# Kernel optimization log

Measured on AMD Instinct MI355X. Metric: run time of the kernel, lower is better.

## Reference

```python
import jax, jax.numpy as jnp
import numpy as np

B, S, D, H, WS = 2, 4096, 768, 12, 256
HD = D // H
NW = S // WS
EPS = 1e-5


def layernorm(x, g, b):
    mu = jnp.mean(x, axis=-1, keepdims=True)
    var = jnp.mean(jnp.square(x - mu), axis=-1, keepdims=True)
    return (x - mu) * jax.lax.rsqrt(var + EPS) * g + b


def setup_inputs() -> dict:
    key = jax.random.key(0)
    ks = jax.random.split(key, 8)
    s = 0.02
    return {
        "x": jax.random.normal(ks[0], (B, S, D), dtype=jnp.float32),
        "Wq": jax.random.normal(ks[1], (D, D), dtype=jnp.float32) * s,
        "bq": jnp.zeros((D,), jnp.float32),
        "Wk": jax.random.normal(ks[2], (D, D), dtype=jnp.float32) * s,
        "bk": jnp.zeros((D,), jnp.float32),
        "Wv": jax.random.normal(ks[3], (D, D), dtype=jnp.float32) * s,
        "bv": jnp.zeros((D,), jnp.float32),
        "Wo": jax.random.normal(ks[4], (D, D), dtype=jnp.float32) * s,
        "bo": jnp.zeros((D,), jnp.float32),
        "ln1_g": jnp.ones((D,), jnp.float32),
        "ln1_b": jnp.zeros((D,), jnp.float32),
        "W1": jax.random.normal(ks[5], (D, 4 * D), dtype=jnp.float32) * s,
        "b1": jnp.zeros((4 * D,), jnp.float32),
        "W2": jax.random.normal(ks[6], (4 * D, D), dtype=jnp.float32) * s,
        "b2": jnp.zeros((D,), jnp.float32),
        "ln2_g": jnp.ones((D,), jnp.float32),
        "ln2_b": jnp.zeros((D,), jnp.float32),
    }


def _attn(h, Wq, bq, Wk, bk, Wv, bv, Wo, bo):
    q = (h @ Wq + bq).reshape(B, S, H, HD)
    k = (h @ Wk + bk).reshape(B, S, H, HD)
    v = (h @ Wv + bv).reshape(B, S, H, HD)
    # split into windows: [B, NW, WS, H, HD]
    kb = k.reshape(B, NW, WS, H, HD)
    vb = v.reshape(B, NW, WS, H, HD)
    qw = jnp.moveaxis(q.reshape(B, NW, WS, H, HD), 1, 0)  # [NW, B, WS, H, HD]
    inv = 1.0 / np.sqrt(HD).astype(np.float32)

    def step(carry, qi_i):
        qi, i = qi_i  # qi: [B, WS, H, HD]
        # per key-window scores: [B, H, NW, WSq, WSk]
        scores = jnp.einsum('bqhd,bjkhd->bhjqk', qi, kb) * inv
        attn = jax.nn.softmax(scores, axis=-1)  # per-block softmax (as in source)
        mask = (jnp.arange(NW) <= i).astype(attn.dtype)  # block-causal, include own window
        attn = attn * mask[None, None, :, None, None]
        ctx = jnp.einsum('bhjqk,bjkhd->bqhd', attn, vb)  # sum over key windows
        return carry, ctx

    _, ctxs = jax.lax.scan(step, None, (qw, jnp.arange(NW)))
    ctx = jnp.moveaxis(ctxs, 0, 1).reshape(B, S, D)
    return ctx @ Wo + bo


def reference(x, Wq, bq, Wk, bk, Wv, bv, Wo, bo, ln1_g, ln1_b, W1, b1, W2, b2, ln2_g, ln2_b):
    attn_out = _attn(layernorm(x, ln1_g, ln1_b), Wq, bq, Wk, bk, Wv, bv, Wo, bo)
    x = x + attn_out
    h2 = layernorm(x, ln2_g, ln2_b)
    ff = jax.nn.gelu(h2 @ W1 + b1, approximate=False) @ W2 + b2
    return x + ff
```

## Files before the change

kernel.cpp:

```cpp
#include <hip/hip_runtime.h>
#include <cstdint>
#include <cstddef>

#define DEV __device__ __forceinline__

typedef unsigned short u16;
typedef unsigned int u32;
typedef __attribute__((ext_vector_type(8))) short s16x8;
typedef __attribute__((ext_vector_type(4))) float f32x4;
typedef __attribute__((ext_vector_type(4))) unsigned int u32x4;

typedef unsigned int u32_as1 __attribute__((address_space(1)));
typedef unsigned int u32_as3 __attribute__((address_space(3)));

DEV u16 f2bf(float f){
  unsigned u = __float_as_uint(f);
  u += 0x7fffu + ((u >> 16) & 1u);
  return (u16)(u >> 16);
}

DEV u32 cvtpk_bf16(float lo, float hi){
  u32 r;
  asm("v_cvt_pk_bf16_f32 %0, %1, %2" : "=v"(r) : "v"(lo), "v"(hi));
  return r;
}

DEV float fexp2(float x){
  float r;
  asm("v_exp_f32 %0, %1" : "=v"(r) : "v"(x));
  return r;
}

DEV float frcp(float x){
  float r;
  asm("v_rcp_f32 %0, %1" : "=v"(r) : "v"(x));
  return r;
}

DEV void gload16(const void* g, void* l){
  __builtin_amdgcn_global_load_lds((const u32_as1*)g, (u32_as3*)l, 16, 0, 0);
}

DEV float gelu_tanh(float x){
  float x2 = x*x;
  float z = 2.3022083f * x * fmaf(x2, 0.044715f, 1.0f);
  z = fminf(z, 100.0f);
  float t = fexp2(z);
  return x * t * frcp(t + 1.0f);
}

template<int NZ>
__global__ __launch_bounds__(256) void wconv_kernel(
    const float* __restrict__ Wa, const float* __restrict__ Wb,
    const float* __restrict__ Wc, const float* __restrict__ Wd,
    u16* __restrict__ Da, u16* __restrict__ Db, u16* __restrict__ Dc, u16* __restrict__ Dd,
    int K, int N){
  __shared__ float tl[32][33];
  int z = (NZ>1) ? blockIdx.z : 0;
  const float* W = (z==0)?Wa:(z==1)?Wb:(z==2)?Wc:Wd;
  u16* Wt = (z==0)?Da:(z==1)?Db:(z==2)?Dc:Dd;
  int tx = threadIdx.x & 31, ty = threadIdx.x >> 5;
  int k0 = blockIdx.x * 32, n0 = blockIdx.y * 32;
  #pragma unroll
  for (int p=0;p<4;p++)
    tl[ty+8*p][tx] = W[(size_t)(k0+ty+8*p)*N + (n0+tx)];
  __syncthreads();
  #pragma unroll
  for (int p=0;p<4;p++){
    int n = ty+8*p;
    Wt[(size_t)(n0+n)*K + (k0+tx)] = f2bf(tl[tx][n]);
  }
}

__global__ __launch_bounds__(256) void ln_kernel(const float* __restrict__ x,
                                                 const float* __restrict__ g,
                                                 const float* __restrict__ bta,
                                                 u16* __restrict__ out){
  int row = blockIdx.x, t = threadIdx.x;
  const float* xr = x + (size_t)row*768;
  float v0 = xr[t], v1 = xr[t+256], v2 = xr[t+512];
  float s = v0+v1+v2, s2 = v0*v0+v1*v1+v2*v2;
  #pragma unroll
  for (int m=1;m<64;m<<=1){ s += __shfl_xor(s,m); s2 += __shfl_xor(s2,m); }
  __shared__ float ls[4], ls2[4];
  int w = t>>6;
  if ((t&63)==0){ ls[w]=s; ls2[w]=s2; }
  __syncthreads();
  s = ls[0]+ls[1]+ls[2]+ls[3]; s2 = ls2[0]+ls2[1]+ls2[2]+ls2[3];
  float mu = s*(1.0f/768.0f);
  float rstd = rsqrtf(s2*(1.0f/768.0f) - mu*mu + 1e-5f);
  u16* orow = out + (size_t)row*768;
  orow[t]     = f2bf((v0-mu)*rstd*g[t]     + bta[t]);
  orow[t+256] = f2bf((v1-mu)*rstd*g[t+256] + bta[t+256]);
  orow[t+512] = f2bf((v2-mu)*rstd*g[t+512] + bta[t+512]);
}

template<bool GELU, bool RES, bool OUTBF16, int BM, bool VPERM=false>
__global__ __launch_bounds__(256) void gemm_kernel(
    const u16* __restrict__ A, const u16* __restrict__ Bt0, size_t btStride,
    const float* __restrict__ bias0, const float* __restrict__ bias1, const float* __restrict__ bias2,
    const float* __restrict__ res, void* __restrict__ out0, size_t outStride,
    int M, int N, int K, float qscale, u32* __restrict__ vtb = nullptr)
{
  constexpr int AM = BM/32;
  __shared__ u16 As[BM*64];
  __shared__ u16 Bs[128*64];
  const int t = threadIdx.x, lane = t & 63, w = t >> 6;
  const int lj = lane & 15, g = lane >> 4;
  const int wm = w >> 1, wn = w & 1;
  const int z = blockIdx.z;
  const u16* Bt = Bt0 + (size_t)z * btStride;
  const float* bias = (z==0) ? bias0 : (z==1 ? bias1 : bias2);
  const u16* Arow = A  + (size_t)blockIdx.x * BM * K;
  const u16* Brow = Bt + (size_t)blockIdx.y * 128 * K;

  f32x4 acc[AM][4];
  #pragma unroll
  for (int a=0;a<AM;a++)
    #pragma unroll
    for (int b=0;b<4;b++){ f32x4 zz = {0.f,0.f,0.f,0.f}; acc[a][b] = zz; }

  for (int kk=0; kk<K; kk+=64){
    #pragma unroll
    for (int cc=0;cc<BM/32;cc++){
      int c = cc*256 + t;
      int row = c>>3, gp = c&7;
      gload16(Arow + (size_t)row*K + kk + ((gp ^ (row&7))<<3),
              (void*)(As + (size_t)(cc*256 + w*64)*8));
    }
    #pragma unroll
    for (int cc=0;cc<4;cc++){
      int c = cc*256 + t;
      int row = c>>3, gp = c&7;
      gload16(Brow + (size_t)row*K + kk + ((gp ^ (row&7))<<3),
              (void*)(Bs + (size_t)(cc*256 + w*64)*8));
    }
    __syncthreads();
    #pragma unroll
    for (int ks=0;ks<2;ks++){
      s16x8 af[AM], bfr[4];
      #pragma unroll
      for (int mt=0;mt<AM;mt++){
        int row = wm*(BM/2)+mt*16+lj;
        af[mt]  = *(const s16x8*)&As[(size_t)row*64 + (((ks*4+g) ^ (lj&7))<<3)];
      }
      #pragma unroll
      for (int nt=0;nt<4;nt++){
        int row = wn*64+nt*16+lj;
        bfr[nt] = *(const s16x8*)&Bs[(size_t)row*64 + (((ks*4+g) ^ (lj&7))<<3)];
      }
      #pragma unroll
      for (int mt=0;mt<AM;mt++)
        #pragma unroll
        for (int nt=0;nt<4;nt++)
          acc[mt][nt] = __builtin_amdgcn_mfma_f32_16x16x32_bf16(af[mt], bfr[nt], acc[mt][nt], 0,0,0);
    }
    __syncthreads();
  }

  const size_t gr0 = (size_t)blockIdx.x*BM + wm*(BM/2);
  const int gc0 = blockIdx.y*128 + wn*64;

  if (VPERM && z == 2){
    const int b_ = (int)(gr0 >> 12);
    const int kt = (int)((gr0 & 4095) >> 6);
    #pragma unroll
    for (int mt2=0; mt2<AM; mt2+=2){
      const u32 gnq = 4*(mt2>>1) + g;
      #pragma unroll
      for (int nt=0;nt<4;nt++){
        int gc = gc0 + nt*16 + lj;
        int hh = gc>>6, dd = gc&63;
        float bv = bias[gc];
        size_t base = ((size_t)(b_*12+hh)*64 + dd)*2048 + (size_t)kt*32 + gnq*4;
        #pragma unroll
        for (int r=0;r<4;r++){
          float ve = acc[mt2][nt][r]   + bv;
          float vo = acc[mt2+1][nt][r] + bv;
          vtb[base + r] = cvtpk_bf16(ve, vo);
        }
      }
    }
    return;
  }

  float* outF = (float*)out0; u16* outB = (u16*)out0;
  if (OUTBF16) outB += (size_t)z*outStride; else outF += (size_t)z*outStride;
  #pragma unroll
  for (int mt=0;mt<AM;mt++)
    #pragma unroll
    for (int nt=0;nt<4;nt++){
      int gc = gc0 + nt*16 + lj;
      float bv = bias[gc];
      #pragma unroll
      for (int r=0;r<4;r++){
        size_t gr = gr0 + mt*16 + g*4 + r;
        float val = acc[mt][nt][r] + bv;
        if (z==0) val *= qscale;
        if (RES)  val += res[gr*(size_t)N + gc];
        if (GELU) val = gelu_tanh(val);
        if (OUTBF16) outB[gr*(size_t)N + gc] = f2bf(val);
        else         outF[gr*(size_t)N + gc] = val;
      }
    }
}

__global__ __launch_bounds__(256,2) void attn_kernel(
    const u16* __restrict__ qb, const u16* __restrict__ kb,
    const u16* __restrict__ vtb, u16* __restrict__ ctx)
{
  __shared__ u16 Ks[256*64];
  __shared__ u16 Vs[64*256];
  const int t = threadIdx.x, lane = t & 63, w = t >> 6;
  const int lj = lane & 15, g = lane >> 4;
  const int bx = blockIdx.x;
  const int pp = bx & 7, qq = (bx >> 3) & 3, bh = bx >> 5;
  const int h = bh % 12, b = bh / 12;
  const size_t seqbase = (size_t)b * 4096;
  const int hoff = h * 64;

  #pragma unroll
  for (int f=0; f<2; f++){
    const int iw = f ? (15 - pp) : pp;
    const int qrow0 = iw*256 + qq*64 + w*16;

    s16x8 qa[2];
    #pragma unroll
    for (int ks=0;ks<2;ks++)
      qa[ks] = *(const s16x8*)(qb + (seqbase + qrow0 + lj)*768 + hoff + ks*32 + g*8);

    f32x4 cacc[4];
    #pragma unroll
    for (int dt=0;dt<4;dt++){ f32x4 zz = {0.f,0.f,0.f,0.f}; cacc[dt] = zz; }

    for (int jw=0; jw<=iw; jw++){
      const u16* kwin = kb + (seqbase + jw*256)*768 + hoff;
      const u16* vtwin = vtb + (size_t)bh*64*4096 + jw*256;

      __syncthreads();
      #pragma unroll
      for (int cc=0;cc<8;cc++){
        int c = cc*256 + t;
        int krow = c>>3, vp = c&7;
        gload16(kwin + (size_t)krow*768 + ((vp ^ (krow&7))<<3),
                (void*)(Ks + (size_t)(cc*256 + w*64)*8));
      }
      #pragma unroll
      for (int cc=0;cc<8;cc++){
        int c = cc*256 + t;
        int d = c>>5, cp = c&31;
        gload16(vtwin + (size_t)d*4096 + ((cp ^ (d&15))<<3),
                (void*)(Vs + (size_t)(cc*256 + w*64)*8));
      }
      __syncthreads();

      f32x4 sacc[16];
      #pragma unroll
      for (int kt=0;kt<16;kt++){ f32x4 zz = {0.f,0.f,0.f,0.f}; sacc[kt] = zz; }
      __builtin_amdgcn_s_setprio(1);
      #pragma unroll
      for (int kt=0;kt<16;kt++){
        int kl = kt*16 + lj;
        #pragma unroll
        for (int ks=0;ks<2;ks++){
          s16x8 kf = *(const s16x8*)&Ks[ (size_t)kl*64 + (((4*ks+g) ^ (kl&7))<<3) ];
          sacc[kt] = __builtin_amdgcn_mfma_f32_16x16x32_bf16(kf, qa[ks], sacc[kt], 0,0,0);
        }
      }
      __builtin_amdgcn_s_setprio(0);

      float sm = 0.f;
      #pragma unroll
      for (int kt=0;kt<16;kt++)
        #pragma unroll
        for (int r=0;r<4;r++){
          float pv = fexp2(sacc[kt][r]);
          sacc[kt][r] = pv; sm += pv;
        }
      sm += __shfl_xor(sm, 16);
      sm += __shfl_xor(sm, 32);
      float rs = frcp(sm);

      f32x4 pacc[4];
      #pragma unroll
      for (int dt=0;dt<4;dt++){ f32x4 zz = {0.f,0.f,0.f,0.f}; pacc[dt] = zz; }
      #pragma unroll
      for (int ks=0;ks<8;ks++){
        u32x4 pw;
        #pragma unroll
        for (int r=0;r<4;r++)
          pw[r] = cvtpk_bf16(sacc[2*ks][r], sacc[2*ks+1][r]);
        s16x8 pa = __builtin_bit_cast(s16x8, pw);
        __builtin_amdgcn_s_setprio(1);
        #pragma unroll
        for (int dt=0;dt<4;dt++){
          int d = dt*16 + lj;
          s16x8 vf = *(const s16x8*)&Vs[ (size_t)d*256 + (((4*ks+g) ^ (d&15))<<3) ];
          pacc[dt] = __builtin_amdgcn_mfma_f32_16x16x32_bf16(pa, vf, pacc[dt], 0,0,0);
        }
        __builtin_amdgcn_s_setprio(0);
      }
      #pragma unroll
      for (int dt=0;dt<4;dt++)
        #pragma unroll
        for (int r=0;r<4;r++)
          cacc[dt][r] += rs * pacc[dt][r];
    }

    #pragma unroll
    for (int dt=0;dt<4;dt++)
      #pragma unroll
      for (int r=0;r<4;r++){
        int qrow = qrow0 + g*4 + r;
        ctx[ (seqbase + qrow)*768 + hoff + dt*16 + lj ] = f2bf(cacc[dt][r]);
      }
  }
}

extern "C" void kernel_launch(void* const* d_in, const int* in_sizes, int n_in,
                              void* d_out, int out_size, void* d_ws, size_t ws_size,
                              hipStream_t stream)
{
  const float* x    = (const float*)d_in[0];
  const float* Wq   = (const float*)d_in[1];
  const float* bq   = (const float*)d_in[2];
  const float* Wk   = (const float*)d_in[3];
  const float* bk   = (const float*)d_in[4];
  const float* Wv   = (const float*)d_in[5];
  const float* bv   = (const float*)d_in[6];
  const float* Wo   = (const float*)d_in[7];
  const float* bo   = (const float*)d_in[8];
  const float* ln1g = (const float*)d_in[9];
  const float* ln1b = (const float*)d_in[10];
  const float* W1   = (const float*)d_in[11];
  const float* b1   = (const float*)d_in[12];
  const float* W2   = (const float*)d_in[13];
  const float* b2   = (const float*)d_in[14];
  const float* ln2g = (const float*)d_in[15];
  const float* ln2b = (const float*)d_in[16];

  char* ws = (char*)d_ws;
  constexpr size_t SZ_W768  = (size_t)768*768*2;
  constexpr size_t SZ_W3072 = (size_t)768*3072*2;
  constexpr size_t SZ_HB    = (size_t)8192*768*2;
  u16* wtq = (u16*)(ws);
  u16* wtk = (u16*)(ws + SZ_W768);
  u16* wtv = (u16*)(ws + 2*SZ_W768);
  u16* wto = (u16*)(ws + 3*SZ_W768);
  u16* wt1 = (u16*)(ws + 4*SZ_W768);
  u16* wt2 = (u16*)(ws + 4*SZ_W768 + SZ_W3072);
  char* p0 = ws + 4*SZ_W768 + 2*SZ_W3072;
  u16*   hbuf  = (u16*)p0;
  u16*   qbuf  = (u16*)(p0 + SZ_HB);
  u16*   kbuf  = (u16*)(p0 + 2*SZ_HB);
  u16*   vtbuf = (u16*)(p0 + 3*SZ_HB);
  u16*   cbuf  = (u16*)(p0 + 4*SZ_HB);
  float* x1    = (float*)(p0 + 5*SZ_HB);
  u16*   ffa   = qbuf;
  float* outp  = (float*)d_out;

  wconv_kernel<4><<<dim3(24,24,4), 256, 0, stream>>>(
      Wq, Wk, Wv, Wo, wtq, wtk, wtv, wto, 768, 768);
  wconv_kernel<1><<<dim3(24,96), 256, 0, stream>>>(
      W1, W1, W1, W1, wt1, wt1, wt1, wt1, 768, 3072);
  wconv_kernel<1><<<dim3(96,24), 256, 0, stream>>>(
      W2, W2, W2, W2, wt2, wt2, wt2, wt2, 3072, 768);

  ln_kernel<<<8192, 256, 0, stream>>>(x, ln1g, ln1b, hbuf);
  gemm_kernel<false,false,true,128,true><<<dim3(64,6,3), 256, 0, stream>>>(
      hbuf, wtq, (size_t)768*768, bq, bk, bv, nullptr, qbuf, (size_t)8192*768,
      8192, 768, 768, 0.180336880111f, (u32*)vtbuf);
  attn_kernel<<<768, 256, 0, stream>>>(qbuf, kbuf, vtbuf, cbuf);
  gemm_kernel<false,true,false,64><<<dim3(128,6,1), 256, 0, stream>>>(
      cbuf, wto, 0, bo, bo, bo, x, x1, 0, 8192, 768, 768, 1.0f);
  ln_kernel<<<8192, 256, 0, stream>>>(x1, ln2g, ln2b, hbuf);
  gemm_kernel<true,false,true,128><<<dim3(64,24,1), 256, 0, stream>>>(
      hbuf, wt1, 0, b1, b1, b1, nullptr, ffa, 0, 8192, 3072, 768, 1.0f);
  gemm_kernel<false,true,false,64><<<dim3(128,6,1), 256, 0, stream>>>(
      ffa, wt2, 0, b2, b2, b2, x1, outp, 0, 8192, 768, 3072, 1.0f);
}
```

Before: 296.4 us.

## Share one LDS buffer for K and V in attention and store residual in bf16

The attention kernel now keeps K and V in a single 32 KB LDS buffer instead of two. V is loaded only after the QK^T MFMAs finish, with extra barriers between phases, and the launch bound is raised to 3 blocks per CU so occupancy can go up. Separately, the post-attention residual x1 is stored as bf16 instead of fp32, and the second layernorm and the final residual add read it as bf16, which halves that tensor's memory traffic. In exchange, the V load can no longer overlap the score computation, and the residual stream loses precision, which may increase numerical error.

```diff
diff --git a/kernel.cpp b/kernel.cpp
--- a/kernel.cpp
+++ b/kernel.cpp
@@ -18,6 +18,8 @@
   u += 0x7fffu + ((u >> 16) & 1u);
   return (u16)(u >> 16);
 }
+
+DEV float bf2f(u16 v){ return __uint_as_float(((u32)v) << 16); }
 
 DEV u32 cvtpk_bf16(float lo, float hi){
   u32 r;
@@ -72,13 +74,20 @@
   }
 }
 
-__global__ __launch_bounds__(256) void ln_kernel(const float* __restrict__ x,
+template<bool INBF16>
+__global__ __launch_bounds__(256) void ln_kernel(const void* __restrict__ xin,
                                                  const float* __restrict__ g,
                                                  const float* __restrict__ bta,
                                                  u16* __restrict__ out){
   int row = blockIdx.x, t = threadIdx.x;
-  const float* xr = x + (size_t)row*768;
-  float v0 = xr[t], v1 = xr[t+256], v2 = xr[t+512];
+  float v0, v1, v2;
+  if (INBF16){
+    const u16* xr = (const u16*)xin + (size_t)row*768;
+    v0 = bf2f(xr[t]); v1 = bf2f(xr[t+256]); v2 = bf2f(xr[t+512]);
+  } else {
+    const float* xr = (const float*)xin + (size_t)row*768;
+    v0 = xr[t]; v1 = xr[t+256]; v2 = xr[t+512];
+  }
   float s = v0+v1+v2, s2 = v0*v0+v1*v1+v2*v2;
   #pragma unroll
   for (int m=1;m<64;m<<=1){ s += __shfl_xor(s,m); s2 += __shfl_xor(s2,m); }
@@ -95,11 +104,11 @@
   orow[t+512] = f2bf((v2-mu)*rstd*g[t+512] + bta[t+512]);
 }
 
-template<bool GELU, bool RES, bool OUTBF16, int BM, bool VPERM=false>
+template<bool GELU, bool RES, bool OUTBF16, int BM, bool VPERM=false, bool RESBF16=false>
 __global__ __launch_bounds__(256) void gemm_kernel(
     const u16* __restrict__ A, const u16* __restrict__ Bt0, size_t btStride,
     const float* __restrict__ bias0, const float* __restrict__ bias1, const float* __restrict__ bias2,
-    const float* __restrict__ res, void* __restrict__ out0, size_t outStride,
+    const void* __restrict__ res, void* __restrict__ out0, size_t outStride,
     int M, int N, int K, float qscale, u32* __restrict__ vtb = nullptr)
 {
   constexpr int AM = BM/32;
@@ -197,7 +206,10 @@
         size_t gr = gr0 + mt*16 + g*4 + r;
         float val = acc[mt][nt][r] + bv;
         if (z==0) val *= qscale;
-        if (RES)  val += res[gr*(size_t)N + gc];
+        if (RES){
+          if (RESBF16) val += bf2f(((const u16*)res)[gr*(size_t)N + gc]);
+          else         val += ((const float*)res)[gr*(size_t)N + gc];
+        }
         if (GELU) val = gelu_tanh(val);
         if (OUTBF16) outB[gr*(size_t)N + gc] = f2bf(val);
         else         outF[gr*(size_t)N + gc] = val;
@@ -205,12 +217,11 @@
     }
 }
 
-__global__ __launch_bounds__(256,2) void attn_kernel(
+__global__ __launch_bounds__(256,3) void attn_kernel(
     const u16* __restrict__ qb, const u16* __restrict__ kb,
     const u16* __restrict__ vtb, u16* __restrict__ ctx)
 {
-  __shared__ u16 Ks[256*64];
-  __shared__ u16 Vs[64*256];
+  __shared__ u16 KV[256*64];
   const int t = threadIdx.x, lane = t & 63, w = t >> 6;
   const int lj = lane & 15, g = lane >> 4;
   const int bx = blockIdx.x;
@@ -243,31 +254,33 @@
         int c = cc*256 + t;
         int krow = c>>3, vp = c&7;
         gload16(kwin + (size_t)krow*768 + ((vp ^ (krow&7))<<3),
-                (void*)(Ks + (size_t)(cc*256 + w*64)*8));
-      }
+                (void*)(KV + (size_t)(cc*256 + w*64)*8));
+      }
+      __syncthreads();
+
+      f32x4 sacc[16];
+      #pragma unroll
+      for (int kt=0;kt<16;kt++){ f32x4 zz = {0.f,0.f,0.f,0.f}; sacc[kt] = zz; }
+      __builtin_amdgcn_s_setprio(1);
+      #pragma unroll
+      for (int kt=0;kt<16;kt++){
+        int kl = kt*16 + lj;
+        #pragma unroll
+        for (int ks=0;ks<2;ks++){
+          s16x8 kf = *(const s16x8*)&KV[ (size_t)kl*64 + (((4*ks+g) ^ (kl&7))<<3) ];
+          sacc[kt] = __builtin_amdgcn_mfma_f32_16x16x32_bf16(kf, qa[ks], sacc[kt], 0,0,0);
+        }
+      }
+      __builtin_amdgcn_s_setprio(0);
+      __syncthreads();
+
       #pragma unroll
       for (int cc=0;cc<8;cc++){
         int c = cc*256 + t;
         int d = c>>5, cp = c&31;
         gload16(vtwin + (size_t)d*4096 + ((cp ^ (d&15))<<3),
-                (void*)(Vs + (size_t)(cc*256 + w*64)*8));
-      }
-      __syncthreads();
-
-      f32x4 sacc[16];
-      #pragma unroll
-      for (int kt=0;kt<16;kt++){ f32x4 zz = {0.f,0.f,0.f,0.f}; sacc[kt] = zz; }
-      __builtin_amdgcn_s_setprio(1);
-      #pragma unroll
-      for (int kt=0;kt<16;kt++){
-        int kl = kt*16 + lj;
-        #pragma unroll
-        for (int ks=0;ks<2;ks++){
-          s16x8 kf = *(const s16x8*)&Ks[ (size_t)kl*64 + (((4*ks+g) ^ (kl&7))<<3) ];
-          sacc[kt] = __builtin_amdgcn_mfma_f32_16x16x32_bf16(kf, qa[ks], sacc[kt], 0,0,0);
-        }
-      }
-      __builtin_amdgcn_s_setprio(0);
+                (void*)(KV + (size_t)(cc*256 + w*64)*8));
+      }
 
       float sm = 0.f;
       #pragma unroll
@@ -280,6 +293,8 @@
       sm += __shfl_xor(sm, 16);
       sm += __shfl_xor(sm, 32);
       float rs = frcp(sm);
+
+      __syncthreads();
 
       f32x4 pacc[4];
       #pragma unroll
@@ -295,7 +310,7 @@
         #pragma unroll
         for (int dt=0;dt<4;dt++){
           int d = dt*16 + lj;
-          s16x8 vf = *(const s16x8*)&Vs[ (size_t)d*256 + (((4*ks+g) ^ (d&15))<<3) ];
+          s16x8 vf = *(const s16x8*)&KV[ (size_t)d*256 + (((4*ks+g) ^ (d&15))<<3) ];
           pacc[dt] = __builtin_amdgcn_mfma_f32_16x16x32_bf16(pa, vf, pacc[dt], 0,0,0);
         }
         __builtin_amdgcn_s_setprio(0);
@@ -355,7 +370,7 @@
   u16*   kbuf  = (u16*)(p0 + 2*SZ_HB);
   u16*   vtbuf = (u16*)(p0 + 3*SZ_HB);
   u16*   cbuf  = (u16*)(p0 + 4*SZ_HB);
-  float* x1    = (float*)(p0 + 5*SZ_HB);
+  u16*   x1    = (u16*)(p0 + 5*SZ_HB);
   u16*   ffa   = qbuf;
   float* outp  = (float*)d_out;
 
@@ -366,16 +381,16 @@
   wconv_kernel<1><<<dim3(96,24), 256, 0, stream>>>(
       W2, W2, W2, W2, wt2, wt2, wt2, wt2, 3072, 768);
 
-  ln_kernel<<<8192, 256, 0, stream>>>(x, ln1g, ln1b, hbuf);
+  ln_kernel<false><<<8192, 256, 0, stream>>>(x, ln1g, ln1b, hbuf);
   gemm_kernel<false,false,true,128,true><<<dim3(64,6,3), 256, 0, stream>>>(
       hbuf, wtq, (size_t)768*768, bq, bk, bv, nullptr, qbuf, (size_t)8192*768,
       8192, 768, 768, 0.180336880111f, (u32*)vtbuf);
   attn_kernel<<<768, 256, 0, stream>>>(qbuf, kbuf, vtbuf, cbuf);
-  gemm_kernel<false,true,false,64><<<dim3(128,6,1), 256, 0, stream>>>(
+  gemm_kernel<false,true,true,64><<<dim3(128,6,1), 256, 0, stream>>>(
       cbuf, wto, 0, bo, bo, bo, x, x1, 0, 8192, 768, 768, 1.0f);
-  ln_kernel<<<8192, 256, 0, stream>>>(x1, ln2g, ln2b, hbuf);
+  ln_kernel<true><<<8192, 256, 0, stream>>>(x1, ln2g, ln2b, hbuf);
   gemm_kernel<true,false,true,128><<<dim3(64,24,1), 256, 0, stream>>>(
       hbuf, wt1, 0, b1, b1, b1, nullptr, ffa, 0, 8192, 3072, 768, 1.0f);
-  gemm_kernel<false,true,false,64><<<dim3(128,6,1), 256, 0, stream>>>(
+  gemm_kernel<false,true,false,64,false,true><<<dim3(128,6,1), 256, 0, stream>>>(
       ffa, wt2, 0, b2, b2, b2, x1, outp, 0, 8192, 768, 3072, 1.0f);
 }
```

New measurement: 275.8 us. 6.9% less time.
